# Kernel tuning notes

Measured on AMD Instinct MI355X. Metric: run time of the kernel, lower is better.

Reference implementation:

```python
import jax, jax.numpy as jnp
import numpy as np

B, T, P, W = 32, 4096, 512, 1024  # batch, time, param_size, width


def setup_inputs() -> dict:
    key = jax.random.key(0)
    ks = jax.random.split(key, 9)
    lim = 1.0 / np.sqrt(W).astype(np.float32)
    lim = float(lim)
    u = lambda k, shape, l: jax.random.uniform(k, shape, minval=-l, maxval=l, dtype=jnp.float32)
    a = jax.random.normal(ks[0], (B, T, P), dtype=jnp.float32)
    h0 = u(ks[1], (W,), lim)
    weight_ih = u(ks[2], (3 * W, P), lim)
    weight_hh = u(ks[3], (3 * W, W), lim)
    bias = u(ks[4], (3 * W,), lim)
    bias_n = u(ks[5], (W,), lim)
    lim_o = float(1.0 / np.sqrt(W))
    w_out = u(ks[6], (P, W), lim_o)
    b_out = u(ks[7], (P,), lim_o)
    return {"a": a, "h0": h0, "weight_ih": weight_ih, "weight_hh": weight_hh,
            "bias": bias, "bias_n": bias_n, "w_out": w_out, "b_out": b_out}


def _encode(a, h0, weight_ih, weight_hh, bias, bias_n, w_out, b_out):
    # Precompute input gates for all steps (big GEMM, hoisted out of the scan).
    # ig: [B, T, 3W]
    ig = jnp.einsum('btp,gp->btg', a, weight_ih) + bias

    def step(h, ig_t):
        # h: [B, W], ig_t: [B, 3W]
        hg = h @ weight_hh.T                       # [B, 3W]
        ig_r, ig_z, ig_n = jnp.split(ig_t, 3, axis=-1)
        hg_r, hg_z, hg_n = jnp.split(hg, 3, axis=-1)
        r = jax.nn.sigmoid(ig_r + hg_r)
        z = jax.nn.sigmoid(ig_z + hg_z)
        n = jnp.tanh(ig_n + r * (hg_n + bias_n))
        h_new = n + z * (h - n)                    # equinox GRUCell update
        return h_new, h_new

    h_init = jnp.broadcast_to(h0, (a.shape[0], h0.shape[0]))
    # scan over time (reverse), batched inside: xs [T, B, 3W]
    _, hs = jax.lax.scan(step, h_init, jnp.swapaxes(ig, 0, 1), reverse=True)
    hs = jnp.swapaxes(hs, 0, 1)                    # [B, T, W]
    return hs @ w_out.T + b_out                    # [B, T, P]


def reference(a, h0, weight_ih, weight_hh, bias, bias_n, w_out, b_out):
    return _encode(a, h0, weight_ih, weight_hh, bias, bias_n, w_out, b_out)
```

## Files before the change

### kernel.cpp

```cpp
#include <hip/hip_runtime.h>
#include <cstddef>

#define TT 4096
#define PP 512
#define WW 1024

using u32 = unsigned;
using u64 = unsigned long long;
using u16 = unsigned short;

typedef short short8 __attribute__((ext_vector_type(8)));
typedef float f32x4 __attribute__((ext_vector_type(4)));

__device__ __forceinline__ u32 bfround(float f) {
    u32 u = __float_as_uint(f);
    return (u + 0x7fffu + ((u >> 16) & 1u)) >> 16;
}
__device__ __forceinline__ float bf2f(u32 q) { return __uint_as_float(q << 16); }
__device__ __forceinline__ float bflo(u32 q) { return __uint_as_float(q << 16); }
__device__ __forceinline__ float bfhi(u32 q) { return __uint_as_float(q & 0xffff0000u); }

#define LDA64(p)    __hip_atomic_load((p),  __ATOMIC_RELAXED, __HIP_MEMORY_SCOPE_AGENT)
#define STA64(p, v) __hip_atomic_store((p), (v), __ATOMIC_RELAXED, __HIP_MEMORY_SCOPE_AGENT)
#define LDA32(p)    __hip_atomic_load((p),  __ATOMIC_RELAXED, __HIP_MEMORY_SCOPE_AGENT)
#define STA32(p, v) __hip_atomic_store((p), (v), __ATOMIC_RELAXED, __HIP_MEMORY_SCOPE_AGENT)
#define STA16(p, v) __hip_atomic_store((p), (v), __ATOMIC_RELAXED, __HIP_MEMORY_SCOPE_AGENT)

__global__ __launch_bounds__(256, 2) void a2bf_t(const float* __restrict__ a,
                                                 u16* __restrict__ abf2) {
    __shared__ u16 sh[32][528];

    const int t   = blockIdx.x;
    const int tid = threadIdx.x;
    {
        const int b = tid >> 3, seg = tid & 7;
        const float* ap = &a[((size_t)b * TT + t) * PP + seg * 64];
        #pragma unroll
        for (int j = 0; j < 16; ++j) {
            float4 v = *(const float4*)&ap[j * 4];
            uint2 w;
            w.x = bfround(v.x) | (bfround(v.y) << 16);
            w.y = bfround(v.z) | (bfround(v.w) << 16);
            *(uint2*)&sh[b][seg * 64 + j * 4] = w;
        }
    }
    __syncthreads();
    {
        const int d = tid >> 2, bq = tid & 3;
        #pragma unroll
        for (int bb = 0; bb < 8; ++bb) {
            const int b = bq * 8 + bb;
            uint4 v = *(const uint4*)&sh[b][d * 8];
            *(uint4*)&abf2[(((size_t)t * 64 + d) * 32 + b) * 8] = v;
        }
    }
}

__global__ __launch_bounds__(768, 1) void ig_prepass10(
    const u16* __restrict__ abf2, const float* __restrict__ Wih,
    const float* __restrict__ bias, char* __restrict__ igbase)
{
    __shared__ __align__(8) u16 sIg[2][32][48];

    const int gWG = blockIdx.x;
    const int t0  = blockIdx.y * 128;
    const int tid = threadIdx.x;
    const int lane = tid & 63;
    const int wid  = tid >> 6;
    const int tpar = wid / 6;
    const int t6   = wid % 6;
    const int st   = t6 >> 1;
    const int bh   = t6 & 1;
    const int lq   = lane >> 4;
    const int bcol = lane & 15;

    short8 af[16];
    float  bi[4];
    {
        const float* wr = &Wih[(size_t)(st * WW + gWG * 16 + bcol) * PP + lq * 8];
        #pragma unroll
        for (int s = 0; s < 16; ++s) {
            float t8[8];
            *(float4*)&t8[0] = *(const float4*)&wr[s * 32];
            *(float4*)&t8[4] = *(const float4*)&wr[s * 32 + 4];
            #pragma unroll
            for (int j = 0; j < 8; ++j) af[s][j] = (short)bfround(t8[j]);
        }
        #pragma unroll
        for (int r = 0; r < 4; ++r) bi[r] = bias[st * WW + gWG * 16 + lq * 4 + r];
    }

    for (int it = 0; it < 64; ++it) {
        const int t = t0 + it * 2 + tpar;
        const u16* bp = &abf2[(((size_t)t * 64 + lq) * 32 + (bh * 16 + bcol)) * 8];
        f32x4 d = {0.f, 0.f, 0.f, 0.f};
        #pragma unroll 4
        for (int s = 0; s < 16; ++s) {
            short8 bf = *(const short8*)&bp[(size_t)s * 4 * 256];
            d = __builtin_amdgcn_mfma_f32_16x16x32_bf16(af[s], bf, d, 0, 0, 0);
        }
        u32 lo = bfround(d[0] + bi[0]) | (bfround(d[1] + bi[1]) << 16);
        u32 hi = bfround(d[2] + bi[2]) | (bfround(d[3] + bi[3]) << 16);
        *(u64*)&sIg[tpar][bh * 16 + bcol][st * 16 + lq * 4] = (u64)lo | ((u64)hi << 32);
        __syncthreads();
        {
            const int tp2 = tid / 384;
            const int off = tid - tp2 * 384;
            const int tt  = t0 + it * 2 + tp2;
            ((u64*)(igbase + ((size_t)tt * 64 + gWG) * 3072))[off] =
                ((const u64*)&sIg[tp2][0][0])[off];
        }
        __syncthreads();
    }
}

__global__ __launch_bounds__(768, 1) void ig_prepass16(
    const float* __restrict__ a, const float* __restrict__ Wih,
    const float* __restrict__ bias, char* __restrict__ igbase)
{
    const int gp   = blockIdx.x;
    const int t0   = blockIdx.y * 64;
    const int tid  = threadIdx.x;
    const int lane = tid & 63;
    const int wid  = tid >> 6;
    const int growb = gp * 192 + wid * 16;

    short8 afrag[16];
    float  biasv[4];
    {
        const float* wr = &Wih[(size_t)(growb + (lane & 15)) * PP + (lane >> 4) * 8];
        #pragma unroll
        for (int s = 0; s < 16; ++s) {
            float t8[8];
            *(float4*)&t8[0] = *(const float4*)&wr[s * 32];
            *(float4*)&t8[4] = *(const float4*)&wr[s * 32 + 4];
            #pragma unroll
            for (int j = 0; j < 8; ++j) afrag[s][j] = (short)bfround(t8[j]);
        }
        #pragma unroll
        for (int r = 0; r < 4; ++r) biasv[r] = bias[growb + (lane >> 4) * 4 + r];
    }
    const int grow0 = growb + (lane >> 4) * 4;
    const int gate  = grow0 >> 10;
    const int w     = grow0 & 1023;
    const int gWG   = w >> 4;
    const int slot  = gate * 16 + (w & 15);
    const int bcol  = lane & 15;

    for (int ct = 0; ct < 128; ++ct) {
        const int t = t0 + (ct >> 1);
        const int b = (ct & 1) * 16 + bcol;
        const float* ap = &a[((size_t)b * TT + t) * PP + (lane >> 4) * 8];
        f32x4 d = {0.f, 0.f, 0.f, 0.f};
        #pragma unroll 4
        for (int s = 0; s < 16; ++s) {
            float4 lo = *(const float4*)&ap[s * 32];
            float4 hi = *(const float4*)&ap[s * 32 + 4];
            short8 bfv;
            bfv[0] = (short)((__float_as_uint(lo.x) + 0x8000u) >> 16);
            bfv[1] = (short)((__float_as_uint(lo.y) + 0x8000u) >> 16);
            bfv[2] = (short)((__float_as_uint(lo.z) + 0x8000u) >> 16);
            bfv[3] = (short)((__float_as_uint(lo.w) + 0x8000u) >> 16);
            bfv[4] = (short)((__float_as_uint(hi.x) + 0x8000u) >> 16);
            bfv[5] = (short)((__float_as_uint(hi.y) + 0x8000u) >> 16);
            bfv[6] = (short)((__float_as_uint(hi.z) + 0x8000u) >> 16);
            bfv[7] = (short)((__float_as_uint(hi.w) + 0x8000u) >> 16);
            d = __builtin_amdgcn_mfma_f32_16x16x32_bf16(afrag[s], bfv, d, 0, 0, 0);
        }
        u32 lo32 = bfround(d[0] + biasv[0]) | (bfround(d[1] + biasv[1]) << 16);
        u32 hi32 = bfround(d[2] + biasv[2]) | (bfround(d[3] + biasv[3]) << 16);
        *(u64*)(igbase + (((size_t)t * 64 + gWG) * 1536 + (size_t)b * 48 + slot) * 2) =
            (u64)lo32 | ((u64)hi32 << 32);
    }
}

__global__ __launch_bounds__(768, 1) void gru_scan5(
    const float* __restrict__ h0v, const float* __restrict__ Whh,
    const float* __restrict__ bias_n, const float* __restrict__ Wout,
    const float* __restrict__ bout, const char* __restrict__ igbase,
    float* __restrict__ out, u64* __restrict__ bufA, u64* __restrict__ bufB,
    u32* __restrict__ flags)
{
    __shared__ float sPreH[4][48][2][17];
    __shared__ float sOutP[4][16][18];
    __shared__ __align__(8) u64 sIgRaw[384];

    const int g    = blockIdx.x;
    const int tid  = threadIdx.x;
    const int lane = tid & 63;
    const int wid  = tid >> 6;
    const int p0   = (g >> 1) * 16;
    const int pb0  = (g & 1) * 16;

    short8 frag[24];
    if (wid < 8) {
        const int kq = wid & 3;
        #pragma unroll
        for (int gate = 0; gate < 3; ++gate)
            #pragma unroll
            for (int s = 0; s < 8; ++s) {
                const float* wr = &Whh[(size_t)(gate * WW + g * 16 + (lane & 15)) * WW
                                       + (kq * 8 + s) * 32 + (lane >> 4) * 8];
                float t8[8];
                *(float4*)&t8[0] = *(const float4*)&wr[0];
                *(float4*)&t8[4] = *(const float4*)&wr[4];
                short8 v;
                #pragma unroll
                for (int j = 0; j < 8; ++j) v[j] = (short)bfround(t8[j]);
                frag[gate * 8 + s] = v;
            }
    } else {
        const int kq3 = wid - 8;
        #pragma unroll
        for (int s = 0; s < 8; ++s) {
            const float* wr = &Wout[(size_t)(p0 + (lane & 15)) * WW
                                    + (kq3 * 8 + s) * 32 + (lane >> 4) * 8];
            float t8[8];
            *(float4*)&t8[0] = *(const float4*)&wr[0];
            *(float4*)&t8[4] = *(const float4*)&wr[4];
            short8 v;
            #pragma unroll
            for (int j = 0; j < 8; ++j) v[j] = (short)bfround(t8[j]);
            frag[s] = v;
        }
    }

    const bool isGate = (tid >= 256 && tid < 384);
    float h_own[4] = {0.f, 0.f, 0.f, 0.f};
    float bnv[4]   = {0.f, 0.f, 0.f, 0.f};
    int   q = 0, b_ = 0;
    u32   pubIdx = 0;
    if (isGate) {
        const int idx = tid - 256;
        q  = idx & 3;
        b_ = idx >> 2;
        #pragma unroll
        for (int j = 0; j < 4; ++j) {
            h_own[j] = h0v[g * 16 + q * 4 + j];
            bnv[j]   = bias_n[g * 16 + q * 4 + j];
        }
        pubIdx = (u32)(g * 128 + 2 * ((q >> 1) * 32 + b_) + (q & 1));
        u32 lo = bfround(h_own[0]) | (bfround(h_own[1]) << 16);
        u32 hi = bfround(h_own[2]) | (bfround(h_own[3]) << 16);
        STA64(&bufA[pubIdx], (u64)lo | ((u64)hi << 32));
    }
    if (wid == 4 || wid == 5) {
        asm volatile("s_waitcnt vmcnt(0)" ::: "memory");
        if (lane == 0) STA32(&flags[g * 16 + (wid - 4)], 1u);
    }

    const float boutp = (tid < 256) ? bout[p0 + (tid & 15)] : 0.f;
    const int fo_hh = (lane >> 4) * 32 + ((wid >> 2) & 1) * 16 + (lane & 15);
    const int fo_p3 = (lane >> 4) * 32 + pb0 + (lane & 15);

    u64* hcur = bufA;
    u64* hnxt = bufB;
    u32 kk = 1;

    for (int t = TT - 1; t >= 0; --t) {
        __syncthreads();

        u64 igr = 0;
        if (tid < 384) igr = *(const u64*)(igbase + ((size_t)t * 64 + g) * 3072 + tid * 8);

        for (;;) {
            u64 v = LDA64((const u64*)&flags[lane * 16]);
            const u32 lo = (u32)v, hi = (u32)(v >> 32);
            if (__all(((int)(lo - kk) >= 0) && ((int)(hi - kk) >= 0))) break;
            __builtin_amdgcn_s_sleep(1);
        }
        asm volatile("" ::: "memory");

        if (wid < 8) {
            const int kq = wid & 3;
            f32x4 c0 = {0.f,0.f,0.f,0.f}, c1 = {0.f,0.f,0.f,0.f}, c2 = {0.f,0.f,0.f,0.f};
            #pragma unroll
            for (int s = 0; s < 8; ++s) {
                const int ss = kq * 8 + s;
                const u64 q0 = LDA64(&hcur[2 * (ss * 128 + fo_hh)]);
                const u64 q1 = LDA64(&hcur[2 * (ss * 128 + fo_hh) + 1]);
                union { u64 qq[2]; short8 v; } uu; uu.qq[0] = q0; uu.qq[1] = q1;
                c0 = __builtin_amdgcn_mfma_f32_16x16x32_bf16(frag[s],      uu.v, c0, 0, 0, 0);
                c1 = __builtin_amdgcn_mfma_f32_16x16x32_bf16(frag[8 + s],  uu.v, c1, 0, 0, 0);
                c2 = __builtin_amdgcn_mfma_f32_16x16x32_bf16(frag[16 + s], uu.v, c2, 0, 0, 0);
            }
            const int bt = wid >> 2, r0 = (lane >> 4) * 4, col = lane & 15;
            #pragma unroll
            for (int r = 0; r < 4; ++r) {
                sPreH[kq][r0 + r][bt][col]      = c0[r];
                sPreH[kq][16 + r0 + r][bt][col] = c1[r];
                sPreH[kq][32 + r0 + r][bt][col] = c2[r];
            }
        } else if (t < TT - 1) {
            const int kq3 = wid - 8;
            f32x4 d = {0.f, 0.f, 0.f, 0.f};
            #pragma unroll
            for (int s = 0; s < 8; ++s) {
                const int ss = kq3 * 8 + s;
                const u64 q0 = LDA64(&hcur[2 * (ss * 128 + fo_p3)]);
                const u64 q1 = LDA64(&hcur[2 * (ss * 128 + fo_p3) + 1]);
                union { u64 qq[2]; short8 v; } uu; uu.qq[0] = q0; uu.qq[1] = q1;
                d = __builtin_amdgcn_mfma_f32_16x16x32_bf16(frag[s], uu.v, d, 0, 0, 0);
            }
            const int r0 = (lane >> 4) * 4, col = lane & 15;
            #pragma unroll
            for (int r = 0; r < 4; ++r) sOutP[kq3][r0 + r][col] = d[r];
        }
        if (tid < 384) sIgRaw[tid] = igr;
        __syncthreads();

        if (isGate) {
            const u16* sIgU = (const u16*)sIgRaw;
            const int bh = b_ >> 4, bc = b_ & 15;
            u32 lo = 0, hi = 0;
            #pragma unroll
            for (int j = 0; j < 4; ++j) {
                const int gwl = q * 4 + j;
                const float ig_r = bf2f(sIgU[b_ * 48 + gwl]);
                const float ig_z = bf2f(sIgU[b_ * 48 + 16 + gwl]);
                const float ig_n = bf2f(sIgU[b_ * 48 + 32 + gwl]);
                const float hg_r = sPreH[0][gwl][bh][bc] + sPreH[1][gwl][bh][bc]
                                 + sPreH[2][gwl][bh][bc] + sPreH[3][gwl][bh][bc];
                const float hg_z = sPreH[0][16 + gwl][bh][bc] + sPreH[1][16 + gwl][bh][bc]
                                 + sPreH[2][16 + gwl][bh][bc] + sPreH[3][16 + gwl][bh][bc];
                const float hg_n = sPreH[0][32 + gwl][bh][bc] + sPreH[1][32 + gwl][bh][bc]
                                 + sPreH[2][32 + gwl][bh][bc] + sPreH[3][32 + gwl][bh][bc];
                const float rr = __builtin_amdgcn_rcpf(1.f + __expf(-(ig_r + hg_r)));
                const float zz = __builtin_amdgcn_rcpf(1.f + __expf(-(ig_z + hg_z)));
                const float xn = ig_n + rr * (hg_n + bnv[j]);
                const float nn = 2.f * __builtin_amdgcn_rcpf(1.f + __expf(-2.f * xn)) - 1.f;
                h_own[j] = nn + zz * (h_own[j] - nn);
                const u32 bv = bfround(h_own[j]);
                if (j == 0) lo = bv;
                else if (j == 1) lo |= bv << 16;
                else if (j == 2) hi = bv;
                else hi |= bv << 16;
            }
            STA64(&hnxt[pubIdx], (u64)lo | ((u64)hi << 32));
        } else if (tid < 256 && t < TT - 1) {
            const int p = tid & 15, b = tid >> 4;
            const float s_ = boutp + sOutP[0][p][b] + sOutP[1][p][b]
                                   + sOutP[2][p][b] + sOutP[3][p][b];
            out[((size_t)(pb0 + b) * TT + (t + 1)) * PP + p0 + p] = s_;
        }
        if (wid == 4 || wid == 5) {
            asm volatile("s_waitcnt vmcnt(0)" ::: "memory");
            if (lane == 0) STA32(&flags[g * 16 + (wid - 4)], kk + 1u);
        }

        u64* tmp = hcur; hcur = hnxt; hnxt = tmp;
        ++kk;
    }

    __syncthreads();
    if (wid >= 8) {
        for (;;) {
            u64 v = LDA64((const u64*)&flags[lane * 16]);
            const u32 lo = (u32)v, hi = (u32)(v >> 32);
            if (__all(((int)(lo - kk) >= 0) && ((int)(hi - kk) >= 0))) break;
            __builtin_amdgcn_s_sleep(1);
        }
        asm volatile("" ::: "memory");
        const int kq3 = wid - 8;
        f32x4 d = {0.f, 0.f, 0.f, 0.f};
        #pragma unroll
        for (int s = 0; s < 8; ++s) {
            const int ss = kq3 * 8 + s;
            const u64 q0 = LDA64(&hcur[2 * (ss * 128 + fo_p3)]);
            const u64 q1 = LDA64(&hcur[2 * (ss * 128 + fo_p3) + 1]);
            union { u64 qq[2]; short8 v; } uu; uu.qq[0] = q0; uu.qq[1] = q1;
            d = __builtin_amdgcn_mfma_f32_16x16x32_bf16(frag[s], uu.v, d, 0, 0, 0);
        }
        const int r0 = (lane >> 4) * 4, col = lane & 15;
        #pragma unroll
        for (int r = 0; r < 4; ++r) sOutP[kq3][r0 + r][col] = d[r];
    }
    __syncthreads();
    if (tid < 256) {
        const int p = tid & 15, b = tid >> 4;
        const float s_ = boutp + sOutP[0][p][b] + sOutP[1][p][b]
                               + sOutP[2][p][b] + sOutP[3][p][b];
        out[((size_t)(pb0 + b) * TT) * PP + p0 + p] = s_;
    }
}

__device__ __forceinline__ void grid_barrier32(u32* leaf, u32* root, u32 rtarget, int g) {
    asm volatile("s_waitcnt vmcnt(0)" ::: "memory");
    __syncthreads();
    if (threadIdx.x == 0) {
        u32 old = __hip_atomic_fetch_add(&leaf[(g & 7) * 16], 1u,
                                         __ATOMIC_RELAXED, __HIP_MEMORY_SCOPE_AGENT);
        if ((old & 31u) == 31u)
            __hip_atomic_fetch_add(root, 1u, __ATOMIC_RELAXED, __HIP_MEMORY_SCOPE_AGENT);
        while (__hip_atomic_load(root, __ATOMIC_RELAXED, __HIP_MEMORY_SCOPE_AGENT) < rtarget)
            __builtin_amdgcn_s_sleep(2);
    }
    __syncthreads();
}

__global__ __launch_bounds__(768, 1) void gru_scan_fb(
    const float* __restrict__ a, const float* __restrict__ h0,
    const float* __restrict__ Wih, const float* __restrict__ Whh,
    const float* __restrict__ bias, const float* __restrict__ bias_n,
    const float* __restrict__ Wout, const float* __restrict__ bout,
    float* __restrict__ out, u64* __restrict__ hbufA, u64* __restrict__ hbufB,
    u32* __restrict__ leaf, u32* __restrict__ root)
{
    __shared__ float sWhh[12][WW];
    __shared__ __align__(16) u64 sh[8192];
    __shared__ float sPreH[2][12][32];
    __shared__ float sIg[2][2][12][32];
    __shared__ float sOutPart[12][64];

    const int g   = blockIdx.x;
    const int tid = threadIdx.x;
    const int w0  = g * 4;

    for (int i = tid; i < 12 * (WW / 4); i += 768) {
        int row_ = i / (WW / 4);
        int k4_  = i - row_ * (WW / 4);
        int gr   = (row_ >> 2) * WW + w0 + (row_ & 3);
        *(float4*)&sWhh[row_][k4_ * 4] = *(const float4*)&Whh[(size_t)gr * WW + k4_ * 4];
    }
    const int  half = (tid >= 384) ? 1 : 0;
    const int  sub  = tid - half * 384;
    const int  b1   = sub & 31;
    const int  row  = sub >> 5;
    const int  grow = (row >> 2) * WW + w0 + (row & 3);
    const float biasv = (half == 0) ? bias[grow] : 0.0f;

    float ho0 = 0.f, ho1 = 0.f, ho2 = 0.f, ho3 = 0.f;
    float bn0 = 0.f, bn1 = 0.f, bn2 = 0.f, bn3 = 0.f;
    if (tid < 32) {
        ho0 = h0[w0 + 0]; ho1 = h0[w0 + 1]; ho2 = h0[w0 + 2]; ho3 = h0[w0 + 3];
        bn0 = bias_n[w0 + 0]; bn1 = bias_n[w0 + 1]; bn2 = bias_n[w0 + 2]; bn3 = bias_n[w0 + 3];
// ... 104 lines not shown
            u32 lo = bfround(hn0) | (bfround(hn1) << 16);
            u32 hi = bfround(hn2) | (bfround(hn3) << 16);
            STA64(&hnxt[g * 32 + tid], (u64)lo | ((u64)hi << 32));
        }
        if (t < TT - 1 && tid < 64) {
            float s_ = boutv;
            #pragma unroll
            for (int cc = 0; cc < 12; ++cc) s_ += sOutPart[cc][o];
            out[((size_t)p3b * TT + (t + 1)) * PP + p3p] = s_;
        }
        rtarget += 8;
        grid_barrier32(leaf, root, rtarget, g);
        u64* tmp = hcur; hcur = hnxt; hnxt = tmp;
    }
    {
        u64 r0, r1, r2, r3, r4, r5, r6, r7, r8, r9, r10 = 0;
        #define LDH(J) LDA64(&hcur[tid + (J) * 768])
        r0 = LDH(0); r1 = LDH(1); r2 = LDH(2); r3 = LDH(3); r4 = LDH(4);
        r5 = LDH(5); r6 = LDH(6); r7 = LDH(7); r8 = LDH(8); r9 = LDH(9);
        if (tid < 512) r10 = LDH(10);
        #undef LDH
        sh[tid] = r0;          sh[tid + 768] = r1;   sh[tid + 1536] = r2;
        sh[tid + 2304] = r3;   sh[tid + 3072] = r4;  sh[tid + 3840] = r5;
        sh[tid + 4608] = r6;   sh[tid + 5376] = r7;  sh[tid + 6144] = r8;
        sh[tid + 6912] = r9;
        if (tid < 512) sh[tid + 7680] = r10;
        __syncthreads();
        p3partials();
        __syncthreads();
        if (tid < 64) {
            float s_ = boutv;
            #pragma unroll
            for (int cc = 0; cc < 12; ++cc) s_ += sOutPart[cc][o];
            out[((size_t)p3b * TT) * PP + p3p] = s_;
        }
    }
}

extern "C" void kernel_launch(void* const* d_in, const int* in_sizes, int n_in,
                              void* d_out, int out_size, void* d_ws, size_t ws_size,
                              hipStream_t stream) {
    const float* a      = (const float*)d_in[0];
    const float* h0     = (const float*)d_in[1];
    const float* Wih    = (const float*)d_in[2];
    const float* Whh    = (const float*)d_in[3];
    const float* bias   = (const float*)d_in[4];
    const float* bias_n = (const float*)d_in[5];
    const float* Wout   = (const float*)d_in[6];
    const float* bout   = (const float*)d_in[7];
    float* out = (float*)d_out;

    const size_t IG_BYTES   = (size_t)TT * 64 * 3072;
    const size_t ABF2_BYTES = (size_t)TT * 64 * 32 * 8 * 2;
    const size_t NEED_FULL  = IG_BYTES + ABF2_BYTES + 2 * 65536 + 4096;
    const size_t NEED_MID   = IG_BYTES + 2 * 65536 + 4096;

    if (ws_size >= NEED_FULL) {
        char* igbase = (char*)d_ws;
        u16*  abf2   = (u16*)((char*)d_ws + IG_BYTES);
        u64*  bufA   = (u64*)((char*)d_ws + IG_BYTES + ABF2_BYTES);
        u64*  bufB   = bufA + 8192;
        u32*  flags  = (u32*)((char*)d_ws + IG_BYTES + ABF2_BYTES + 2 * 65536);
        hipMemsetAsync(flags, 0, 4096, stream);
        hipLaunchKernelGGL(a2bf_t, dim3(TT), dim3(256), 0, stream, a, abf2);
        hipLaunchKernelGGL(ig_prepass10, dim3(64, 32), dim3(768), 0, stream,
                           abf2, Wih, bias, igbase);
        void* args[] = {(void*)&h0, (void*)&Whh, (void*)&bias_n, (void*)&Wout,
                        (void*)&bout, (void*)&igbase, (void*)&out,
                        (void*)&bufA, (void*)&bufB, (void*)&flags};
        hipLaunchCooperativeKernel((void*)gru_scan5, dim3(64), dim3(768),
                                   args, 0, stream);
    } else if (ws_size >= NEED_MID) {
        char* igbase = (char*)d_ws;
        u64*  bufA   = (u64*)((char*)d_ws + IG_BYTES);
        u64*  bufB   = bufA + 8192;
        u32*  flags  = (u32*)((char*)d_ws + IG_BYTES + 2 * 65536);
        hipMemsetAsync(flags, 0, 4096, stream);
        hipLaunchKernelGGL(ig_prepass16, dim3(16, 64), dim3(768), 0, stream,
                           a, Wih, bias, igbase);
        void* args[] = {(void*)&h0, (void*)&Whh, (void*)&bias_n, (void*)&Wout,
                        (void*)&bout, (void*)&igbase, (void*)&out,
                        (void*)&bufA, (void*)&bufB, (void*)&flags};
        hipLaunchCooperativeKernel((void*)gru_scan5, dim3(64), dim3(768),
                                   args, 0, stream);
    } else {
        u64* hA   = (u64*)d_ws;
        u64* hB   = hA + 8192;
        u32* leaf = (u32*)((char*)d_ws + 2 * 65536);
        u32* root = leaf + 8 * 16;
        hipMemsetAsync(leaf, 0, 1024, stream);
        void* args[] = {(void*)&a, (void*)&h0, (void*)&Wih, (void*)&Whh,
                        (void*)&bias, (void*)&bias_n, (void*)&Wout, (void*)&bout,
                        (void*)&out, (void*)&hA, (void*)&hB, (void*)&leaf, (void*)&root};
        hipLaunchCooperativeKernel((void*)gru_scan_fb, dim3(256), dim3(768),
                                   args, 0, stream);
    }
}
```

Baseline: 20.93 ms.

## Double-buffer prepass smem, prefetch next-step ig, spread gate work over more threads

```diff
diff --git a/kernel.cpp b/kernel.cpp
--- a/kernel.cpp
+++ b/kernel.cpp
@@ -24,7 +24,6 @@
 #define STA64(p, v) __hip_atomic_store((p), (v), __ATOMIC_RELAXED, __HIP_MEMORY_SCOPE_AGENT)
 #define LDA32(p)    __hip_atomic_load((p),  __ATOMIC_RELAXED, __HIP_MEMORY_SCOPE_AGENT)
 #define STA32(p, v) __hip_atomic_store((p), (v), __ATOMIC_RELAXED, __HIP_MEMORY_SCOPE_AGENT)
-#define STA16(p, v) __hip_atomic_store((p), (v), __ATOMIC_RELAXED, __HIP_MEMORY_SCOPE_AGENT)
 
 __global__ __launch_bounds__(256, 2) void a2bf_t(const float* __restrict__ a,
                                                  u16* __restrict__ abf2) {
@@ -60,7 +59,7 @@
     const u16* __restrict__ abf2, const float* __restrict__ Wih,
     const float* __restrict__ bias, char* __restrict__ igbase)
 {
-    __shared__ __align__(8) u16 sIg[2][32][48];
+    __shared__ __align__(8) u16 sIg[2][2][32][48];
 
     const int gWG = blockIdx.x;
     const int t0  = blockIdx.y * 128;
@@ -91,6 +90,7 @@
     }
 
     for (int it = 0; it < 64; ++it) {
+        const int par = it & 1;
         const int t = t0 + it * 2 + tpar;
         const u16* bp = &abf2[(((size_t)t * 64 + lq) * 32 + (bh * 16 + bcol)) * 8];
         f32x4 d = {0.f, 0.f, 0.f, 0.f};
@@ -101,16 +101,15 @@
         }
         u32 lo = bfround(d[0] + bi[0]) | (bfround(d[1] + bi[1]) << 16);
         u32 hi = bfround(d[2] + bi[2]) | (bfround(d[3] + bi[3]) << 16);
-        *(u64*)&sIg[tpar][bh * 16 + bcol][st * 16 + lq * 4] = (u64)lo | ((u64)hi << 32);
+        *(u64*)&sIg[par][tpar][bh * 16 + bcol][st * 16 + lq * 4] = (u64)lo | ((u64)hi << 32);
         __syncthreads();
         {
             const int tp2 = tid / 384;
             const int off = tid - tp2 * 384;
             const int tt  = t0 + it * 2 + tp2;
             ((u64*)(igbase + ((size_t)tt * 64 + gWG) * 3072))[off] =
-                ((const u64*)&sIg[tp2][0][0])[off];
-        }
-        __syncthreads();
+                ((const u64*)&sIg[par][tp2][0][0])[off];
+        }
     }
 }
 
@@ -174,7 +173,7 @@
     }
 }
 
-__global__ __launch_bounds__(768, 1) void gru_scan5(
+__global__ __launch_bounds__(768, 1) void gru_scan6(
     const float* __restrict__ h0v, const float* __restrict__ Whh,
     const float* __restrict__ bias_n, const float* __restrict__ Wout,
     const float* __restrict__ bout, const char* __restrict__ igbase,
@@ -225,26 +224,21 @@
         }
     }
 
-    const bool isGate = (tid >= 256 && tid < 384);
-    float h_own[4] = {0.f, 0.f, 0.f, 0.f};
-    float bnv[4]   = {0.f, 0.f, 0.f, 0.f};
-    int   q = 0, b_ = 0;
-    u32   pubIdx = 0;
+    const bool isGate = (tid >= 256 && tid < 512);
+    float hA_ = 0.f, hB_ = 0.f, bnA = 0.f, bnB = 0.f;
+    int   v = 0, b_ = 0;
+    u32   pubU = 0;
     if (isGate) {
-        const int idx = tid - 256;
-        q  = idx & 3;
-        b_ = idx >> 2;
-        #pragma unroll
-        for (int j = 0; j < 4; ++j) {
-            h_own[j] = h0v[g * 16 + q * 4 + j];
-            bnv[j]   = bias_n[g * 16 + q * 4 + j];
-        }
-        pubIdx = (u32)(g * 128 + 2 * ((q >> 1) * 32 + b_) + (q & 1));
-        u32 lo = bfround(h_own[0]) | (bfround(h_own[1]) << 16);
-        u32 hi = bfround(h_own[2]) | (bfround(h_own[3]) << 16);
-        STA64(&bufA[pubIdx], (u64)lo | ((u64)hi << 32));
-    }
-    if (wid == 4 || wid == 5) {
+        const int u = tid - 256;
+        const int v3 = u >> 7, bit2 = (u >> 1) & 1, bit1 = u & 1;
+        b_ = (u >> 2) & 31;
+        v  = 8 * v3 + 4 * bit2 + 2 * bit1;
+        hA_ = h0v[g * 16 + v];     hB_ = h0v[g * 16 + v + 1];
+        bnA = bias_n[g * 16 + v];  bnB = bias_n[g * 16 + v + 1];
+        pubU = (u32)(g * 256 + u);
+        STA32(&((u32*)bufA)[pubU], bfround(hA_) | (bfround(hB_) << 16));
+    }
+    if (wid >= 4 && wid < 8) {
         asm volatile("s_waitcnt vmcnt(0)" ::: "memory");
         if (lane == 0) STA32(&flags[g * 16 + (wid - 4)], 1u);
     }
@@ -253,6 +247,11 @@
     const int fo_hh = (lane >> 4) * 32 + ((wid >> 2) & 1) * 16 + (lane & 15);
     const int fo_p3 = (lane >> 4) * 32 + pb0 + (lane & 15);
 
+    const bool isLd = (tid >= 512) || (tid < 128);
+    const int  li   = (tid >= 512) ? (tid - 512) : (tid + 256);
+    u64 igr_cur = 0;
+    if (isLd) igr_cur = *(const u64*)(igbase + ((size_t)(TT - 1) * 64 + g) * 3072 + li * 8);
+
     u64* hcur = bufA;
     u64* hnxt = bufB;
     u32 kk = 1;
@@ -260,13 +259,14 @@
     for (int t = TT - 1; t >= 0; --t) {
         __syncthreads();
 
-        u64 igr = 0;
-        if (tid < 384) igr = *(const u64*)(igbase + ((size_t)t * 64 + g) * 3072 + tid * 8);
-
         for (;;) {
-            u64 v = LDA64((const u64*)&flags[lane * 16]);
-            const u32 lo = (u32)v, hi = (u32)(v >> 32);
-            if (__all(((int)(lo - kk) >= 0) && ((int)(hi - kk) >= 0))) break;
+            u64 f0 = LDA64((const u64*)&flags[lane * 16]);
+            u64 f1 = LDA64((const u64*)&flags[lane * 16 + 2]);
+            const u32 a0 = (u32)f0, a1 = (u32)(f0 >> 32);
+            const u32 a2 = (u32)f1, a3 = (u32)(f1 >> 32);
+            const bool ok = ((int)(a0 - kk) >= 0) && ((int)(a1 - kk) >= 0) &&
+                            ((int)(a2 - kk) >= 0) && ((int)(a3 - kk) >= 0);
+            if (__all(ok)) break;
             __builtin_amdgcn_s_sleep(1);
         }
         asm volatile("" ::: "memory");
@@ -279,10 +279,10 @@
                 const int ss = kq * 8 + s;
                 const u64 q0 = LDA64(&hcur[2 * (ss * 128 + fo_hh)]);
                 const u64 q1 = LDA64(&hcur[2 * (ss * 128 + fo_hh) + 1]);
-                union { u64 qq[2]; short8 v; } uu; uu.qq[0] = q0; uu.qq[1] = q1;
-                c0 = __builtin_amdgcn_mfma_f32_16x16x32_bf16(frag[s],      uu.v, c0, 0, 0, 0);
-                c1 = __builtin_amdgcn_mfma_f32_16x16x32_bf16(frag[8 + s],  uu.v, c1, 0, 0, 0);
-                c2 = __builtin_amdgcn_mfma_f32_16x16x32_bf16(frag[16 + s], uu.v, c2, 0, 0, 0);
+                union { u64 qq[2]; short8 vv; } uu; uu.qq[0] = q0; uu.qq[1] = q1;
+                c0 = __builtin_amdgcn_mfma_f32_16x16x32_bf16(frag[s],      uu.vv, c0, 0, 0, 0);
+                c1 = __builtin_amdgcn_mfma_f32_16x16x32_bf16(frag[8 + s],  uu.vv, c1, 0, 0, 0);
+                c2 = __builtin_amdgcn_mfma_f32_16x16x32_bf16(frag[16 + s], uu.vv, c2, 0, 0, 0);
             }
             const int bt = wid >> 2, r0 = (lane >> 4) * 4, col = lane & 15;
             #pragma unroll
@@ -299,23 +299,26 @@
                 const int ss = kq3 * 8 + s;
                 const u64 q0 = LDA64(&hcur[2 * (ss * 128 + fo_p3)]);
                 const u64 q1 = LDA64(&hcur[2 * (ss * 128 + fo_p3) + 1]);
-                union { u64 qq[2]; short8 v; } uu; uu.qq[0] = q0; uu.qq[1] = q1;
-                d = __builtin_amdgcn_mfma_f32_16x16x32_bf16(frag[s], uu.v, d, 0, 0, 0);
+                union { u64 qq[2]; short8 vv; } uu; uu.qq[0] = q0; uu.qq[1] = q1;
+                d = __builtin_amdgcn_mfma_f32_16x16x32_bf16(frag[s], uu.vv, d, 0, 0, 0);
             }
             const int r0 = (lane >> 4) * 4, col = lane & 15;
             #pragma unroll
             for (int r = 0; r < 4; ++r) sOutP[kq3][r0 + r][col] = d[r];
         }
-        if (tid < 384) sIgRaw[tid] = igr;
+        if (isLd) {
+            sIgRaw[li] = igr_cur;
+            if (t > 0)
+                igr_cur = *(const u64*)(igbase + ((size_t)(t - 1) * 64 + g) * 3072 + li * 8);
+        }
         __syncthreads();
 
         if (isGate) {
             const u16* sIgU = (const u16*)sIgRaw;
             const int bh = b_ >> 4, bc = b_ & 15;
-            u32 lo = 0, hi = 0;
-            #pragma unroll
-            for (int j = 0; j < 4; ++j) {
-                const int gwl = q * 4 + j;
+            u32 pk;
+            {
+                const int gwl = v;
                 const float ig_r = bf2f(sIgU[b_ * 48 + gwl]);
                 const float ig_z = bf2f(sIgU[b_ * 48 + 16 + gwl]);
                 const float ig_n = bf2f(sIgU[b_ * 48 + 32 + gwl]);
@@ -327,23 +330,37 @@
                                  + sPreH[2][32 + gwl][bh][bc] + sPreH[3][32 + gwl][bh][bc];
                 const float rr = __builtin_amdgcn_rcpf(1.f + __expf(-(ig_r + hg_r)));
                 const float zz = __builtin_amdgcn_rcpf(1.f + __expf(-(ig_z + hg_z)));
-                const float xn = ig_n + rr * (hg_n + bnv[j]);
+                const float xn = ig_n + rr * (hg_n + bnA);
                 const float nn = 2.f * __builtin_amdgcn_rcpf(1.f + __expf(-2.f * xn)) - 1.f;
-                h_own[j] = nn + zz * (h_own[j] - nn);
-                const u32 bv = bfround(h_own[j]);
-                if (j == 0) lo = bv;
-                else if (j == 1) lo |= bv << 16;
-                else if (j == 2) hi = bv;
-                else hi |= bv << 16;
-            }
-            STA64(&hnxt[pubIdx], (u64)lo | ((u64)hi << 32));
+                hA_ = nn + zz * (hA_ - nn);
+                pk = bfround(hA_);
+            }
+            {
+                const int gwl = v + 1;
+                const float ig_r = bf2f(sIgU[b_ * 48 + gwl]);
+                const float ig_z = bf2f(sIgU[b_ * 48 + 16 + gwl]);
+                const float ig_n = bf2f(sIgU[b_ * 48 + 32 + gwl]);
+                const float hg_r = sPreH[0][gwl][bh][bc] + sPreH[1][gwl][bh][bc]
+                                 + sPreH[2][gwl][bh][bc] + sPreH[3][gwl][bh][bc];
+                const float hg_z = sPreH[0][16 + gwl][bh][bc] + sPreH[1][16 + gwl][bh][bc]
+                                 + sPreH[2][16 + gwl][bh][bc] + sPreH[3][16 + gwl][bh][bc];
+                const float hg_n = sPreH[0][32 + gwl][bh][bc] + sPreH[1][32 + gwl][bh][bc]
+                                 + sPreH[2][32 + gwl][bh][bc] + sPreH[3][32 + gwl][bh][bc];
+                const float rr = __builtin_amdgcn_rcpf(1.f + __expf(-(ig_r + hg_r)));
+                const float zz = __builtin_amdgcn_rcpf(1.f + __expf(-(ig_z + hg_z)));
+                const float xn = ig_n + rr * (hg_n + bnB);
+                const float nn = 2.f * __builtin_amdgcn_rcpf(1.f + __expf(-2.f * xn)) - 1.f;
+                hB_ = nn + zz * (hB_ - nn);
+                pk |= bfround(hB_) << 16;
+            }
+            STA32(&((u32*)hnxt)[pubU], pk);
         } else if (tid < 256 && t < TT - 1) {
             const int p = tid & 15, b = tid >> 4;
             const float s_ = boutp + sOutP[0][p][b] + sOutP[1][p][b]
                                    + sOutP[2][p][b] + sOutP[3][p][b];
             out[((size_t)(pb0 + b) * TT + (t + 1)) * PP + p0 + p] = s_;
         }
-        if (wid == 4 || wid == 5) {
+        if (wid >= 4 && wid < 8) {
             asm volatile("s_waitcnt vmcnt(0)" ::: "memory");
             if (lane == 0) STA32(&flags[g * 16 + (wid - 4)], kk + 1u);
         }
@@ -353,14 +370,18 @@
     }
 
     __syncthreads();
+    for (;;) {
+        u64 f0 = LDA64((const u64*)&flags[lane * 16]);
+        u64 f1 = LDA64((const u64*)&flags[lane * 16 + 2]);
+        const u32 a0 = (u32)f0, a1 = (u32)(f0 >> 32);
+        const u32 a2 = (u32)f1, a3 = (u32)(f1 >> 32);
+        const bool ok = ((int)(a0 - kk) >= 0) && ((int)(a1 - kk) >= 0) &&
+                        ((int)(a2 - kk) >= 0) && ((int)(a3 - kk) >= 0);
+        if (__all(ok)) break;
+        __builtin_amdgcn_s_sleep(1);
+    }
+    asm volatile("" ::: "memory");
     if (wid >= 8) {
-        for (;;) {
-            u64 v = LDA64((const u64*)&flags[lane * 16]);
-            const u32 lo = (u32)v, hi = (u32)(v >> 32);
-            if (__all(((int)(lo - kk) >= 0) && ((int)(hi - kk) >= 0))) break;
-            __builtin_amdgcn_s_sleep(1);
-        }
-        asm volatile("" ::: "memory");
         const int kq3 = wid - 8;
         f32x4 d = {0.f, 0.f, 0.f, 0.f};
         #pragma unroll
@@ -368,8 +389,8 @@
             const int ss = kq3 * 8 + s;
             const u64 q0 = LDA64(&hcur[2 * (ss * 128 + fo_p3)]);
             const u64 q1 = LDA64(&hcur[2 * (ss * 128 + fo_p3) + 1]);
-            union { u64 qq[2]; short8 v; } uu; uu.qq[0] = q0; uu.qq[1] = q1;
-            d = __builtin_amdgcn_mfma_f32_16x16x32_bf16(frag[s], uu.v, d, 0, 0, 0);
+            union { u64 qq[2]; short8 vv; } uu; uu.qq[0] = q0; uu.qq[1] = q1;
+            d = __builtin_amdgcn_mfma_f32_16x16x32_bf16(frag[s], uu.vv, d, 0, 0, 0);
         }
         const int r0 = (lane >> 4) * 4, col = lane & 15;
         #pragma unroll
@@ -607,7 +628,7 @@
         void* args[] = {(void*)&h0, (void*)&Whh, (void*)&bias_n, (void*)&Wout,
                         (void*)&bout, (void*)&igbase, (void*)&out,
                         (void*)&bufA, (void*)&bufB, (void*)&flags};
-        hipLaunchCooperativeKernel((void*)gru_scan5, dim3(64), dim3(768),
+        hipLaunchCooperativeKernel((void*)gru_scan6, dim3(64), dim3(768),
                                    args, 0, stream);
     } else if (ws_size >= NEED_MID) {
         char* igbase = (char*)d_ws;
@@ -620,7 +641,7 @@
         void* args[] = {(void*)&h0, (void*)&Whh, (void*)&bias_n, (void*)&Wout,
                         (void*)&bout, (void*)&igbase, (void*)&out,
                         (void*)&bufA, (void*)&bufB, (void*)&flags};
-        hipLaunchCooperativeKernel((void*)gru_scan5, dim3(64), dim3(768),
+        hipLaunchCooperativeKernel((void*)gru_scan6, dim3(64), dim3(768),
                                    args, 0, stream);
     } else {
         u64* hA   = (u64*)d_ws;
```

New measurement: 20.85 ms. About the same (-0.4%).

## Split GRU scan batch into two independent halves with separate buffers and flags

Applied to the files above, without the earlier changes.

```diff
diff --git a/kernel.cpp b/kernel.cpp
--- a/kernel.cpp
+++ b/kernel.cpp
@@ -29,9 +29,7 @@
 __global__ __launch_bounds__(256, 2) void a2bf_t(const float* __restrict__ a,
                                                  u16* __restrict__ abf2) {
     __shared__ u16 sh[32][528];
-
-    const int t   = blockIdx.x;
-    const int tid = threadIdx.x;
+    const int t = blockIdx.x, tid = threadIdx.x;
     {
         const int b = tid >> 3, seg = tid & 7;
         const float* ap = &a[((size_t)b * TT + t) * PP + seg * 64];
@@ -60,8 +58,7 @@
     const u16* __restrict__ abf2, const float* __restrict__ Wih,
     const float* __restrict__ bias, char* __restrict__ igbase)
 {
-    __shared__ __align__(8) u16 sIg[2][32][48];
-
+    __shared__ __align__(8) u16 sIg[2][2][32][48];
     const int gWG = blockIdx.x;
     const int t0  = blockIdx.y * 128;
     const int tid = threadIdx.x;
@@ -91,6 +88,7 @@
     }
 
     for (int it = 0; it < 64; ++it) {
+        const int par = it & 1;
         const int t = t0 + it * 2 + tpar;
         const u16* bp = &abf2[(((size_t)t * 64 + lq) * 32 + (bh * 16 + bcol)) * 8];
         f32x4 d = {0.f, 0.f, 0.f, 0.f};
@@ -101,16 +99,15 @@
         }
         u32 lo = bfround(d[0] + bi[0]) | (bfround(d[1] + bi[1]) << 16);
         u32 hi = bfround(d[2] + bi[2]) | (bfround(d[3] + bi[3]) << 16);
-        *(u64*)&sIg[tpar][bh * 16 + bcol][st * 16 + lq * 4] = (u64)lo | ((u64)hi << 32);
+        *(u64*)&sIg[par][tpar][bh * 16 + bcol][st * 16 + lq * 4] = (u64)lo | ((u64)hi << 32);
         __syncthreads();
         {
             const int tp2 = tid / 384;
             const int off = tid - tp2 * 384;
             const int tt  = t0 + it * 2 + tp2;
             ((u64*)(igbase + ((size_t)tt * 64 + gWG) * 3072))[off] =
-                ((const u64*)&sIg[tp2][0][0])[off];
-        }
-        __syncthreads();
+                ((const u64*)&sIg[par][tp2][0][0])[off];
+        }
     }
 }
 
@@ -174,14 +171,16 @@
     }
 }
 
-__global__ __launch_bounds__(768, 1) void gru_scan5(
+__global__ __launch_bounds__(768, 1) void gru_scan7(
     const float* __restrict__ h0v, const float* __restrict__ Whh,
     const float* __restrict__ bias_n, const float* __restrict__ Wout,
     const float* __restrict__ bout, const char* __restrict__ igbase,
-    float* __restrict__ out, u64* __restrict__ bufA, u64* __restrict__ bufB,
-    u32* __restrict__ flags)
+    float* __restrict__ out,
+    u64* __restrict__ bufA0, u64* __restrict__ bufA1,
+    u64* __restrict__ bufB0, u64* __restrict__ bufB1,
+    u32* __restrict__ flagsA, u32* __restrict__ flagsB)
 {
-    __shared__ float sPreH[4][48][2][17];
+    __shared__ float sPreH[8][48][17];
     __shared__ float sOutP[4][16][18];
     __shared__ __align__(8) u64 sIgRaw[384];
 
@@ -190,31 +189,30 @@
     const int lane = tid & 63;
     const int wid  = tid >> 6;
     const int p0   = (g >> 1) * 16;
-    const int pb0  = (g & 1) * 16;
-
-    short8 frag[24];
+    const int cp3  = g & 1;
+
+    short8 frag[12];
     if (wid < 8) {
-        const int kq = wid & 3;
         #pragma unroll
         for (int gate = 0; gate < 3; ++gate)
             #pragma unroll
-            for (int s = 0; s < 8; ++s) {
+            for (int s = 0; s < 4; ++s) {
+                const int ss = wid * 4 + s;
                 const float* wr = &Whh[(size_t)(gate * WW + g * 16 + (lane & 15)) * WW
-                                       + (kq * 8 + s) * 32 + (lane >> 4) * 8];
+                                       + ss * 32 + (lane >> 4) * 8];
                 float t8[8];
                 *(float4*)&t8[0] = *(const float4*)&wr[0];
                 *(float4*)&t8[4] = *(const float4*)&wr[4];
                 short8 v;
                 #pragma unroll
                 for (int j = 0; j < 8; ++j) v[j] = (short)bfround(t8[j]);
-                frag[gate * 8 + s] = v;
+                frag[gate * 4 + s] = v;
             }
     } else {
-        const int kq3 = wid - 8;
         #pragma unroll
         for (int s = 0; s < 8; ++s) {
-            const float* wr = &Wout[(size_t)(p0 + (lane & 15)) * WW
-                                    + (kq3 * 8 + s) * 32 + (lane >> 4) * 8];
+            const int ss = (wid - 8) * 8 + s;
+            const float* wr = &Wout[(size_t)(p0 + (lane & 15)) * WW + ss * 32 + (lane >> 4) * 8];
             float t8[8];
             *(float4*)&t8[0] = *(const float4*)&wr[0];
             *(float4*)&t8[4] = *(const float4*)&wr[4];
@@ -225,162 +223,152 @@
         }
     }
 
-    const bool isGate = (tid >= 256 && tid < 384);
-    float h_own[4] = {0.f, 0.f, 0.f, 0.f};
-    float bnv[4]   = {0.f, 0.f, 0.f, 0.f};
-    int   q = 0, b_ = 0;
-    u32   pubIdx = 0;
+    const bool isGate = (tid >= 256 && tid < 512);
+    const int idx = tid - 256;
+    const int gwl = idx & 15, gb = idx >> 4;
+    float hA = 0.f, hB = 0.f, bnv = 0.f;
+    u32 pidx = 0;
     if (isGate) {
-        const int idx = tid - 256;
-        q  = idx & 3;
-        b_ = idx >> 2;
-        #pragma unroll
-        for (int j = 0; j < 4; ++j) {
-            h_own[j] = h0v[g * 16 + q * 4 + j];
-            bnv[j]   = bias_n[g * 16 + q * 4 + j];
-        }
-        pubIdx = (u32)(g * 128 + 2 * ((q >> 1) * 32 + b_) + (q & 1));
-        u32 lo = bfround(h_own[0]) | (bfround(h_own[1]) << 16);
-        u32 hi = bfround(h_own[2]) | (bfround(h_own[3]) << 16);
-        STA64(&bufA[pubIdx], (u64)lo | ((u64)hi << 32));
-    }
-    if (wid == 4 || wid == 5) {
+        const int w_abs = g * 16 + gwl;
+        hA = h0v[w_abs]; hB = hA;
+        bnv = bias_n[w_abs];
+        pidx = (u32)((((w_abs >> 3) * 16) + gb) * 8 + (w_abs & 7));
+        STA16(&((u16*)bufA0)[pidx], (u16)bfround(hA));
+        STA16(&((u16*)bufB0)[pidx], (u16)bfround(hB));
+    }
+    if (wid >= 4 && wid < 8) {
         asm volatile("s_waitcnt vmcnt(0)" ::: "memory");
-        if (lane == 0) STA32(&flags[g * 16 + (wid - 4)], 1u);
-    }
-
+        if (lane == 0) {
+            STA32(&flagsA[g * 16 + (wid - 4)], 1u);
+            STA32(&flagsB[g * 16 + (wid - 4)], 1u);
+        }
+    }
     const float boutp = (tid < 256) ? bout[p0 + (tid & 15)] : 0.f;
-    const int fo_hh = (lane >> 4) * 32 + ((wid >> 2) & 1) * 16 + (lane & 15);
-    const int fo_p3 = (lane >> 4) * 32 + pb0 + (lane & 15);
-
-    u64* hcur = bufA;
-    u64* hnxt = bufB;
-    u32 kk = 1;
-
-    for (int t = TT - 1; t >= 0; --t) {
-        __syncthreads();
-
-        u64 igr = 0;
-        if (tid < 384) igr = *(const u64*)(igbase + ((size_t)t * 64 + g) * 3072 + tid * 8);
-
+
+    auto poll = [&](u32* flg, u32 want) {
         for (;;) {
-            u64 v = LDA64((const u64*)&flags[lane * 16]);
-            const u32 lo = (u32)v, hi = (u32)(v >> 32);
-            if (__all(((int)(lo - kk) >= 0) && ((int)(hi - kk) >= 0))) break;
+            u64 f0 = LDA64((const u64*)&flg[lane * 16]);
+            u64 f1 = LDA64((const u64*)&flg[lane * 16 + 2]);
+            const u32 a0 = (u32)f0, a1 = (u32)(f0 >> 32);
+            const u32 a2 = (u32)f1, a3 = (u32)(f1 >> 32);
+            const bool ok = ((int)(a0 - want) >= 0) && ((int)(a1 - want) >= 0) &&
+                            ((int)(a2 - want) >= 0) && ((int)(a3 - want) >= 0);
+            if (__all(ok)) break;
             __builtin_amdgcn_s_sleep(1);
         }
         asm volatile("" ::: "memory");
-
-        if (wid < 8) {
-            const int kq = wid & 3;
-            f32x4 c0 = {0.f,0.f,0.f,0.f}, c1 = {0.f,0.f,0.f,0.f}, c2 = {0.f,0.f,0.f,0.f};
-            #pragma unroll
-            for (int s = 0; s < 8; ++s) {
-                const int ss = kq * 8 + s;
-                const u64 q0 = LDA64(&hcur[2 * (ss * 128 + fo_hh)]);
-                const u64 q1 = LDA64(&hcur[2 * (ss * 128 + fo_hh) + 1]);
-                union { u64 qq[2]; short8 v; } uu; uu.qq[0] = q0; uu.qq[1] = q1;
-                c0 = __builtin_amdgcn_mfma_f32_16x16x32_bf16(frag[s],      uu.v, c0, 0, 0, 0);
-                c1 = __builtin_amdgcn_mfma_f32_16x16x32_bf16(frag[8 + s],  uu.v, c1, 0, 0, 0);
-                c2 = __builtin_amdgcn_mfma_f32_16x16x32_bf16(frag[16 + s], uu.v, c2, 0, 0, 0);
-            }
-            const int bt = wid >> 2, r0 = (lane >> 4) * 4, col = lane & 15;
-            #pragma unroll
-            for (int r = 0; r < 4; ++r) {
-                sPreH[kq][r0 + r][bt][col]      = c0[r];
-                sPreH[kq][16 + r0 + r][bt][col] = c1[r];
-                sPreH[kq][32 + r0 + r][bt][col] = c2[r];
-            }
-        } else if (t < TT - 1) {
-            const int kq3 = wid - 8;
-            f32x4 d = {0.f, 0.f, 0.f, 0.f};
-            #pragma unroll
-            for (int s = 0; s < 8; ++s) {
-                const int ss = kq3 * 8 + s;
-                const u64 q0 = LDA64(&hcur[2 * (ss * 128 + fo_p3)]);
-                const u64 q1 = LDA64(&hcur[2 * (ss * 128 + fo_p3) + 1]);
-                union { u64 qq[2]; short8 v; } uu; uu.qq[0] = q0; uu.qq[1] = q1;
-                d = __builtin_amdgcn_mfma_f32_16x16x32_bf16(frag[s], uu.v, d, 0, 0, 0);
-            }
-            const int r0 = (lane >> 4) * 4, col = lane & 15;
-            #pragma unroll
-            for (int r = 0; r < 4; ++r) sOutP[kq3][r0 + r][col] = d[r];
-        }
-        if (tid < 384) sIgRaw[tid] = igr;
-        __syncthreads();
-
+    };
+
+    auto hh = [&](const u64* cur) {
+        f32x4 c0 = {0.f,0.f,0.f,0.f}, c1 = {0.f,0.f,0.f,0.f}, c2 = {0.f,0.f,0.f,0.f};
+        #pragma unroll
+        for (int s = 0; s < 4; ++s) {
+            const int ss = wid * 4 + s;
+            const int base = 2 * (ss * 64 + (lane >> 4) * 16 + (lane & 15));
+            const u64 q0 = LDA64(&cur[base]);
+            const u64 q1 = LDA64(&cur[base + 1]);
+            union { u64 q[2]; short8 v; } uu; uu.q[0] = q0; uu.q[1] = q1;
+            c0 = __builtin_amdgcn_mfma_f32_16x16x32_bf16(frag[s],     uu.v, c0, 0, 0, 0);
+            c1 = __builtin_amdgcn_mfma_f32_16x16x32_bf16(frag[4 + s], uu.v, c1, 0, 0, 0);
+            c2 = __builtin_amdgcn_mfma_f32_16x16x32_bf16(frag[8 + s], uu.v, c2, 0, 0, 0);
+        }
+        const int r0 = (lane >> 4) * 4, col = lane & 15;
+        #pragma unroll
+        for (int r = 0; r < 4; ++r) {
+            sPreH[wid][r0 + r][col]      = c0[r];
+            sPreH[wid][16 + r0 + r][col] = c1[r];
+            sPreH[wid][32 + r0 + r][col] = c2[r];
+        }
+    };
+
+    auto p3c = [&](const u64* cur) {
+        f32x4 d = {0.f, 0.f, 0.f, 0.f};
+        #pragma unroll
+        for (int s = 0; s < 8; ++s) {
+            const int ss = (wid - 8) * 8 + s;
+            const int base = 2 * (ss * 64 + (lane >> 4) * 16 + (lane & 15));
+            const u64 q0 = LDA64(&cur[base]);
+            const u64 q1 = LDA64(&cur[base + 1]);
+            union { u64 q[2]; short8 v; } uu; uu.q[0] = q0; uu.q[1] = q1;
+            d = __builtin_amdgcn_mfma_f32_16x16x32_bf16(frag[s], uu.v, d, 0, 0, 0);
+        }
+        const int r0 = (lane >> 4) * 4, col = lane & 15;
+        #pragma unroll
+        for (int r = 0; r < 4; ++r) sOutP[wid - 8][r0 + r][col] = d[r];
+    };
+
+    auto gates = [&](u64* nxt, float& h_own, int bb, int cb, bool p3own,
+                     u32* flg, u32 kkflag, int t) {
         if (isGate) {
             const u16* sIgU = (const u16*)sIgRaw;
-            const int bh = b_ >> 4, bc = b_ & 15;
-            u32 lo = 0, hi = 0;
+            const float ig_r = bf2f(sIgU[bb * 48 + gwl]);
+            const float ig_z = bf2f(sIgU[bb * 48 + 16 + gwl]);
+            const float ig_n = bf2f(sIgU[bb * 48 + 32 + gwl]);
+            float hg_r = 0.f, hg_z = 0.f, hg_n = 0.f;
             #pragma unroll
-            for (int j = 0; j < 4; ++j) {
-                const int gwl = q * 4 + j;
-                const float ig_r = bf2f(sIgU[b_ * 48 + gwl]);
-                const float ig_z = bf2f(sIgU[b_ * 48 + 16 + gwl]);
-                const float ig_n = bf2f(sIgU[b_ * 48 + 32 + gwl]);
-                const float hg_r = sPreH[0][gwl][bh][bc] + sPreH[1][gwl][bh][bc]
-                                 + sPreH[2][gwl][bh][bc] + sPreH[3][gwl][bh][bc];
-                const float hg_z = sPreH[0][16 + gwl][bh][bc] + sPreH[1][16 + gwl][bh][bc]
-                                 + sPreH[2][16 + gwl][bh][bc] + sPreH[3][16 + gwl][bh][bc];
-                const float hg_n = sPreH[0][32 + gwl][bh][bc] + sPreH[1][32 + gwl][bh][bc]
-                                 + sPreH[2][32 + gwl][bh][bc] + sPreH[3][32 + gwl][bh][bc];
-                const float rr = __builtin_amdgcn_rcpf(1.f + __expf(-(ig_r + hg_r)));
-                const float zz = __builtin_amdgcn_rcpf(1.f + __expf(-(ig_z + hg_z)));
-                const float xn = ig_n + rr * (hg_n + bnv[j]);
-                const float nn = 2.f * __builtin_amdgcn_rcpf(1.f + __expf(-2.f * xn)) - 1.f;
-                h_own[j] = nn + zz * (h_own[j] - nn);
-                const u32 bv = bfround(h_own[j]);
-                if (j == 0) lo = bv;
-                else if (j == 1) lo |= bv << 16;
-                else if (j == 2) hi = bv;
-                else hi |= bv << 16;
+            for (int qz = 0; qz < 8; ++qz) {
+                hg_r += sPreH[qz][gwl][gb];
+                hg_z += sPreH[qz][16 + gwl][gb];
+                hg_n += sPreH[qz][32 + gwl][gb];
             }
-            STA64(&hnxt[pubIdx], (u64)lo | ((u64)hi << 32));
-        } else if (tid < 256 && t < TT - 1) {
+            const float rr = __builtin_amdgcn_rcpf(1.f + __expf(-(ig_r + hg_r)));
+            const float zz = __builtin_amdgcn_rcpf(1.f + __expf(-(ig_z + hg_z)));
+            const float xn = ig_n + rr * (hg_n + bnv);
+            const float nn = 2.f * __builtin_amdgcn_rcpf(1.f + __expf(-2.f * xn)) - 1.f;
+            h_own = nn + zz * (h_own - nn);
+            STA16(&((u16*)nxt)[pidx], (u16)bfround(h_own));
+        } else if (tid < 256 && p3own && t < TT - 1) {
             const int p = tid & 15, b = tid >> 4;
             const float s_ = boutp + sOutP[0][p][b] + sOutP[1][p][b]
                                    + sOutP[2][p][b] + sOutP[3][p][b];
-            out[((size_t)(pb0 + b) * TT + (t + 1)) * PP + p0 + p] = s_;
-        }
-        if (wid == 4 || wid == 5) {
+            out[((size_t)(cb + b) * TT + (t + 1)) * PP + p0 + p] = s_;
+        }
+        if (wid >= 4 && wid < 8) {
             asm volatile("s_waitcnt vmcnt(0)" ::: "memory");
-            if (lane == 0) STA32(&flags[g * 16 + (wid - 4)], kk + 1u);
-        }
-
-        u64* tmp = hcur; hcur = hnxt; hnxt = tmp;
+            if (lane == 0) STA32(&flg[g * 16 + (wid - 4)], kkflag);
+        }
+    };
+
+    u64 *curA = bufA0, *nxtA = bufA1, *curB = bufB0, *nxtB = bufB1;
+    u32 kk = 1;
+
+    for (int t = TT - 1; t >= 0; --t) {
+        u64 igr = 0;
+        if (tid < 384) igr = *(const u64*)(igbase + ((size_t)t * 64 + g) * 3072 + tid * 8);
+
+        poll(flagsA, kk);
+        if (wid < 8) hh(curA);
+        else if (cp3 == 0 && t < TT - 1) p3c(curA);
+        if (tid < 384) sIgRaw[tid] = igr;
+        __syncthreads();
+        gates(nxtA, hA, gb, 0, cp3 == 0, flagsA, kk + 1, t);
+        __syncthreads();
+
+        poll(flagsB, kk);
+        if (wid < 8) hh(curB);
+        else if (cp3 == 1 && t < TT - 1) p3c(curB);
+        __syncthreads();
+        gates(nxtB, hB, 16 + gb, 16, cp3 == 1, flagsB, kk + 1, t);
+        __syncthreads();
+
+        u64* tm;
+        tm = curA; curA = nxtA; nxtA = tm;
+        tm = curB; curB = nxtB; nxtB = tm;
         ++kk;
     }
 
-    __syncthreads();
-    if (wid >= 8) {
-        for (;;) {
-            u64 v = LDA64((const u64*)&flags[lane * 16]);
-            const u32 lo = (u32)v, hi = (u32)(v >> 32);
-            if (__all(((int)(lo - kk) >= 0) && ((int)(hi - kk) >= 0))) break;
-            __builtin_amdgcn_s_sleep(1);
-        }
-        asm volatile("" ::: "memory");
-        const int kq3 = wid - 8;
-        f32x4 d = {0.f, 0.f, 0.f, 0.f};
-        #pragma unroll
-        for (int s = 0; s < 8; ++s) {
-            const int ss = kq3 * 8 + s;
-            const u64 q0 = LDA64(&hcur[2 * (ss * 128 + fo_p3)]);
-            const u64 q1 = LDA64(&hcur[2 * (ss * 128 + fo_p3) + 1]);
-            union { u64 qq[2]; short8 v; } uu; uu.qq[0] = q0; uu.qq[1] = q1;
-            d = __builtin_amdgcn_mfma_f32_16x16x32_bf16(frag[s], uu.v, d, 0, 0, 0);
-        }
-        const int r0 = (lane >> 4) * 4, col = lane & 15;
-        #pragma unroll
-        for (int r = 0; r < 4; ++r) sOutP[kq3][r0 + r][col] = d[r];
-    }
-    __syncthreads();
-    if (tid < 256) {
-        const int p = tid & 15, b = tid >> 4;
-        const float s_ = boutp + sOutP[0][p][b] + sOutP[1][p][b]
-                               + sOutP[2][p][b] + sOutP[3][p][b];
-        out[((size_t)(pb0 + b) * TT) * PP + p0 + p] = s_;
+    {
+        u64* cure = cp3 ? curB : curA;
+        u32* flge = cp3 ? flagsB : flagsA;
+        poll(flge, kk);
+        if (wid >= 8) p3c(cure);
+        __syncthreads();
+        if (tid < 256) {
+            const int p = tid & 15, b = tid >> 4;
+            const float s_ = boutp + sOutP[0][p][b] + sOutP[1][p][b]
+                                   + sOutP[2][p][b] + sOutP[3][p][b];
+            out[((size_t)(cp3 * 16 + b) * TT) * PP + p0 + p] = s_;
+        }
     }
 }
 
@@ -591,36 +579,47 @@
 
     const size_t IG_BYTES   = (size_t)TT * 64 * 3072;
     const size_t ABF2_BYTES = (size_t)TT * 64 * 32 * 8 * 2;
-    const size_t NEED_FULL  = IG_BYTES + ABF2_BYTES + 2 * 65536 + 4096;
-    const size_t NEED_MID   = IG_BYTES + 2 * 65536 + 4096;
+    const size_t BUF_BYTES  = 32768;
+    const size_t NEED_FULL  = IG_BYTES + ABF2_BYTES + 4 * BUF_BYTES + 8192;
+    const size_t NEED_MID   = IG_BYTES + 4 * BUF_BYTES + 8192;
 
     if (ws_size >= NEED_FULL) {
         char* igbase = (char*)d_ws;
         u16*  abf2   = (u16*)((char*)d_ws + IG_BYTES);
-        u64*  bufA   = (u64*)((char*)d_ws + IG_BYTES + ABF2_BYTES);
-        u64*  bufB   = bufA + 8192;
-        u32*  flags  = (u32*)((char*)d_ws + IG_BYTES + ABF2_BYTES + 2 * 65536);
-        hipMemsetAsync(flags, 0, 4096, stream);
+        char* bufs   = (char*)d_ws + IG_BYTES + ABF2_BYTES;
+        u64*  bufA0  = (u64*)(bufs);
+        u64*  bufA1  = (u64*)(bufs + BUF_BYTES);
+        u64*  bufB0  = (u64*)(bufs + 2 * BUF_BYTES);
+        u64*  bufB1  = (u64*)(bufs + 3 * BUF_BYTES);
+        u32*  flagsA = (u32*)(bufs + 4 * BUF_BYTES);
+        u32*  flagsB = flagsA + 1024;
+        hipMemsetAsync(flagsA, 0, 8192, stream);
         hipLaunchKernelGGL(a2bf_t, dim3(TT), dim3(256), 0, stream, a, abf2);
         hipLaunchKernelGGL(ig_prepass10, dim3(64, 32), dim3(768), 0, stream,
                            abf2, Wih, bias, igbase);
         void* args[] = {(void*)&h0, (void*)&Whh, (void*)&bias_n, (void*)&Wout,
                         (void*)&bout, (void*)&igbase, (void*)&out,
-                        (void*)&bufA, (void*)&bufB, (void*)&flags};
-        hipLaunchCooperativeKernel((void*)gru_scan5, dim3(64), dim3(768),
+                        (void*)&bufA0, (void*)&bufA1, (void*)&bufB0, (void*)&bufB1,
+                        (void*)&flagsA, (void*)&flagsB};
+        hipLaunchCooperativeKernel((void*)gru_scan7, dim3(64), dim3(768),
                                    args, 0, stream);
     } else if (ws_size >= NEED_MID) {
         char* igbase = (char*)d_ws;
-        u64*  bufA   = (u64*)((char*)d_ws + IG_BYTES);
-        u64*  bufB   = bufA + 8192;
-        u32*  flags  = (u32*)((char*)d_ws + IG_BYTES + 2 * 65536);
-        hipMemsetAsync(flags, 0, 4096, stream);
+        char* bufs   = (char*)d_ws + IG_BYTES;
+        u64*  bufA0  = (u64*)(bufs);
+        u64*  bufA1  = (u64*)(bufs + BUF_BYTES);
+        u64*  bufB0  = (u64*)(bufs + 2 * BUF_BYTES);
+        u64*  bufB1  = (u64*)(bufs + 3 * BUF_BYTES);
+        u32*  flagsA = (u32*)(bufs + 4 * BUF_BYTES);
+        u32*  flagsB = flagsA + 1024;
+        hipMemsetAsync(flagsA, 0, 8192, stream);
         hipLaunchKernelGGL(ig_prepass16, dim3(16, 64), dim3(768), 0, stream,
                            a, Wih, bias, igbase);
         void* args[] = {(void*)&h0, (void*)&Whh, (void*)&bias_n, (void*)&Wout,
                         (void*)&bout, (void*)&igbase, (void*)&out,
-                        (void*)&bufA, (void*)&bufB, (void*)&flags};
-        hipLaunchCooperativeKernel((void*)gru_scan5, dim3(64), dim3(768),
+                        (void*)&bufA0, (void*)&bufA1, (void*)&bufB0, (void*)&bufB1,
+                        (void*)&flagsA, (void*)&flagsB};
+        hipLaunchCooperativeKernel((void*)gru_scan7, dim3(64), dim3(768),
                                    args, 0, stream);
     } else {
         u64* hA   = (u64*)d_ws;
```

New measurement: 29.12 ms. 39.1% more time.
